# Performance work log

Measured on AMD Instinct MI355X. Metric: run time of the kernel, lower is better.

Reference implementation:

```python
import jax, jax.numpy as jnp
import numpy as np

B, L, F_, T = 64, 49, 2048, 32
V, E, H, A = 15000, 512, 512, 512

def _w(key, shape, scale=0.02):
    return (scale * jax.random.normal(key, shape)).astype(jnp.float32)

def setup_inputs() -> dict:
    key = jax.random.key(0)
    ks = jax.random.split(key, 24)
    inp = {
        "features": jax.random.normal(ks[0], (B, L, F_), dtype=jnp.float32),
        "captions": jax.random.randint(ks[1], (B, T), 0, V),
        "force_prob": 1,
        # parameters (torch nn.Linear convention: W [out,in])
        "init_h_W": _w(ks[2], (H, F_)), "init_h_b": jnp.zeros((H,), jnp.float32),
        "init_c_W": _w(ks[3], (H, F_)), "init_c_b": jnp.zeros((H,), jnp.float32),
        "W_a_W": _w(ks[4], (A, F_)), "W_a_b": jnp.zeros((A,), jnp.float32),
        "U_a_W": _w(ks[5], (A, H)), "U_a_b": jnp.zeros((A,), jnp.float32),
        "v_a_W": _w(ks[6], (1, A)), "v_a_b": jnp.zeros((1,), jnp.float32),
        "embed_table": _w(ks[7], (V, E), 1.0),
        "lstm_W_ih": _w(ks[8], (4 * H, E + F_)), "lstm_W_hh": _w(ks[9], (4 * H, H)),
        "lstm_b_ih": jnp.zeros((4 * H,), jnp.float32), "lstm_b_hh": jnp.zeros((4 * H,), jnp.float32),
        "fc_W": _w(ks[10], (V, H)), "fc_b": jnp.zeros((V,), jnp.float32),
    }
    return inp

def _decoder(features, captions,
             init_h_W, init_h_b, init_c_W, init_c_b,
             W_a_W, W_a_b, U_a_W, U_a_b, v_a_W, v_a_b,
             embed_table, lstm_W_ih, lstm_W_hh, lstm_b_ih, lstm_b_hh,
             fc_W, fc_b):
    emb = embed_table[captions]                      # [B,T,E]
    mean_f = jnp.mean(features, axis=1)              # [B,F]
    h0 = mean_f @ init_h_W.T + init_h_b              # [B,H]
    c0 = mean_f @ init_c_W.T + init_c_b
    # features are constant over time -> precompute W_a(features) once
    att1 = jnp.einsum('blf,af->bla', features, W_a_W) + W_a_b  # [B,L,A]

    def step(carry, w_emb):
        h, c = carry
        att2 = h @ U_a_W.T + U_a_b                   # [B,A]
        score = jnp.tanh(att1 + att2[:, None, :]) @ v_a_W[0] + v_a_b[0]  # [B,L]
        w = jax.nn.softmax(score, axis=1)            # [B,L]
        context = jnp.einsum('bl,blf->bf', w, features)  # [B,F]
        x = jnp.concatenate([w_emb, context], axis=1)     # [B,E+F]
        gates = x @ lstm_W_ih.T + lstm_b_ih + h @ lstm_W_hh.T + lstm_b_hh
        i, f, g, o = jnp.split(gates, 4, axis=1)
        i, f, o = jax.nn.sigmoid(i), jax.nn.sigmoid(f), jax.nn.sigmoid(o)
        g = jnp.tanh(g)
        c_new = f * c + i * g
        h_new = o * jnp.tanh(c_new)                  # dropout p=0 (eval) = identity
        logits = h_new @ fc_W.T + fc_b               # [B,V]
        return (h_new, c_new), logits

    _, logits = jax.lax.scan(step, (h0, c0), jnp.swapaxes(emb, 0, 1))  # [T,B,V]
    return jnp.transpose(logits, (1, 0, 2))          # [B,T,V]

def reference(features, captions, force_prob,
              init_h_W, init_h_b, init_c_W, init_c_b,
              W_a_W, W_a_b, U_a_W, U_a_b, v_a_W, v_a_b,
              embed_table, lstm_W_ih, lstm_W_hh, lstm_b_ih, lstm_b_hh,
              fc_W, fc_b):
    # force_prob == 1 -> teacher forcing at every step (sampling branch never taken)
    return _decoder(features, captions,
                    init_h_W, init_h_b, init_c_W, init_c_b,
                    W_a_W, W_a_b, U_a_W, U_a_b, v_a_W, v_a_b,
                    embed_table, lstm_W_ih, lstm_W_hh, lstm_b_ih, lstm_b_hh,
                    fc_W, fc_b)
```

## Files before the change

kernel.cpp:

```cpp
#include <hip/hip_runtime.h>
#include <math.h>

#define B_ 64
#define L_ 49
#define F_DIM 2048
#define T_ 32
#define V_ 15000
#define E_ 512
#define H_ 512
#define A_ 512

typedef __attribute__((ext_vector_type(8))) short s16x8;
typedef __attribute__((ext_vector_type(4))) short s16x4;
typedef __attribute__((ext_vector_type(4))) float f32x4;

__device__ __forceinline__ unsigned short f2b(float x) {
    union { float f; unsigned int u; } v; v.f = x;
    unsigned int r = v.u + 0x7FFF + ((v.u >> 16) & 1);
    return (unsigned short)(r >> 16);
}
__device__ __forceinline__ float b2f(unsigned short u) {
    union { unsigned int i; float f; } v; v.i = ((unsigned int)u) << 16; return v.f;
}
__device__ __forceinline__ float rcp_fast(float x) {
    return __builtin_amdgcn_rcpf(x);
}
__device__ __forceinline__ float tanhf_fast(float x) {
    x = fminf(fmaxf(x, -15.f), 15.f);
    const float e = __expf(2.f * x);
    return (e - 1.f) * rcp_fast(e + 1.f);
}
__device__ __forceinline__ float sigmoid_fast(float x) {
    return rcp_fast(1.f + __expf(-x));
}

__device__ __forceinline__ float aload_f(const float* p) {
    return __hip_atomic_load((const float*)p, __ATOMIC_RELAXED, __HIP_MEMORY_SCOPE_AGENT);
}
__device__ __forceinline__ void astore_f(float* p, float v) {
    __hip_atomic_store(p, v, __ATOMIC_RELAXED, __HIP_MEMORY_SCOPE_AGENT);
}
__device__ __forceinline__ unsigned long long aload_u64(const void* p) {
    return __hip_atomic_load((const unsigned long long*)p, __ATOMIC_RELAXED, __HIP_MEMORY_SCOPE_AGENT);
}
__device__ __forceinline__ void astore_u32(void* p, unsigned v) {
    __hip_atomic_store((unsigned*)p, v, __ATOMIC_RELAXED, __HIP_MEMORY_SCOPE_AGENT);
}
__device__ __forceinline__ unsigned apoll(const unsigned* p) {
    return __hip_atomic_load(p, __ATOMIC_RELAXED, __HIP_MEMORY_SCOPE_AGENT);
}
__device__ __forceinline__ void abump(unsigned* p) {
    __hip_atomic_fetch_add(p, 1u, __ATOMIC_RELAXED, __HIP_MEMORY_SCOPE_AGENT);
}
__device__ __forceinline__ void aset(unsigned* p, unsigned v) {
    __hip_atomic_store(p, v, __ATOMIC_RELAXED, __HIP_MEMORY_SCOPE_AGENT);
}

__global__ __launch_bounds__(256)
void k_castall(const float* __restrict__ feat, const float* __restrict__ W_a,
               const float* __restrict__ W_ih, const float* __restrict__ fc_W,
               unsigned short* __restrict__ feat_bf,
               unsigned short* __restrict__ wcomb_bf,
               unsigned short* __restrict__ fcW_bf)
{
    const int r  = blockIdx.y;
    const int c4 = blockIdx.x * 256 + threadIdx.x;
    const float* src;
    unsigned short* dst;
    int cols;
    if (r < 3136)      { src = feat + (size_t)r * 2048;                 dst = feat_bf + (size_t)r * 2048;            cols = 2048; }
    else if (r < 3648) { const int rr = r - 3136; src = W_a + (size_t)rr * 2048;              dst = wcomb_bf + (size_t)rr * 2048;          cols = 2048; }
    else if (r < 5696) { const int rr = r - 3648; src = W_ih + (size_t)rr * 2560 + 512;       dst = wcomb_bf + (size_t)(rr + 512) * 2048;  cols = 2048; }
    else               { const int rr = r - 5696; src = fc_W + (size_t)rr * 512;              dst = fcW_bf + (size_t)rr * 512;             cols = 512; }
    if (c4 * 4 >= cols) return;
    float4 v = *reinterpret_cast<const float4*>(src + c4 * 4);
    ushort4 o;
    o.x = f2b(v.x); o.y = f2b(v.y); o.z = f2b(v.z); o.w = f2b(v.w);
    *reinterpret_cast<ushort4*>(dst + c4 * 4) = o;
}

#define LDSW 40
__global__ __launch_bounds__(256)
void gemm_mfma(const unsigned short* __restrict__ A, int lda,
               const void* __restrict__ W0p, int ldw0, int N0,
               const void* __restrict__ W1p, int ldw1, int w32,
               const float* __restrict__ bias0, const float* __restrict__ bias1,
               float* __restrict__ C, int ldc,
               int M, int N, int K, int permT, int obf)
{
    __shared__ unsigned short As[128 * LDSW];
    __shared__ unsigned short Ws[128 * LDSW];

    const int tid  = threadIdx.x;
    const int m0   = blockIdx.x * 128;
    const int n0   = blockIdx.y * 128;
    const int wave = tid >> 6;
    const int lane = tid & 63;
    const int wr   = (wave >> 1) * 64;
    const int wc   = (wave & 1) * 64;

    f32x4 acc[4][4];
    #pragma unroll
    for (int i = 0; i < 4; ++i)
        #pragma unroll
        for (int j = 0; j < 4; ++j)
            acc[i][j] = (f32x4)(0.f);

    const int fr = lane & 15;
    const int fk = (lane >> 4) * 8;

    for (int kc = 0; kc < K; kc += 32) {
        ushort4 av[2][2], wv[2][2];
        #pragma unroll
        for (int i = 0; i < 2; ++i) {
            const int idx = tid + i * 256;
            const int row = idx >> 2;
            const int seg = idx & 3;
            av[i][0] = make_ushort4(0, 0, 0, 0); av[i][1] = make_ushort4(0, 0, 0, 0);
            wv[i][0] = make_ushort4(0, 0, 0, 0); wv[i][1] = make_ushort4(0, 0, 0, 0);
            if (m0 + row < M) {
                const float4 t0 = *reinterpret_cast<const float4*>(
                    A + (size_t)(m0 + row) * lda + kc + seg * 8);
                *reinterpret_cast<float4*>(&av[i][0]) = t0;
            }
            const int n_abs = n0 + row;
            if (n_abs < N) {
                if (w32) {
                    const float* wrow = (n_abs < N0)
                        ? ((const float*)W0p + (size_t)n_abs * ldw0)
                        : ((const float*)W1p + (size_t)(n_abs - N0) * ldw1);
                    const float4 x = *reinterpret_cast<const float4*>(wrow + kc + seg * 8);
                    const float4 y = *reinterpret_cast<const float4*>(wrow + kc + seg * 8 + 4);
                    wv[i][0] = make_ushort4(f2b(x.x), f2b(x.y), f2b(x.z), f2b(x.w));
                    wv[i][1] = make_ushort4(f2b(y.x), f2b(y.y), f2b(y.z), f2b(y.w));
                } else {
                    const unsigned short* wrow = (n_abs < N0)
                        ? ((const unsigned short*)W0p + (size_t)n_abs * ldw0)
                        : ((const unsigned short*)W1p + (size_t)(n_abs - N0) * ldw1);
                    const float4 t0 = *reinterpret_cast<const float4*>(wrow + kc + seg * 8);
                    *reinterpret_cast<float4*>(&wv[i][0]) = t0;
                }
            }
        }
        __syncthreads();
        #pragma unroll
        for (int i = 0; i < 2; ++i) {
            const int idx = tid + i * 256;
            const int row = idx >> 2;
            const int seg = idx & 3;
            *reinterpret_cast<ushort4*>(&As[row * LDSW + seg * 8])     = av[i][0];
            *reinterpret_cast<ushort4*>(&As[row * LDSW + seg * 8 + 4]) = av[i][1];
            *reinterpret_cast<ushort4*>(&Ws[row * LDSW + seg * 8])     = wv[i][0];
            *reinterpret_cast<ushort4*>(&Ws[row * LDSW + seg * 8 + 4]) = wv[i][1];
        }
        __syncthreads();

        s16x8 afr[4], bfr[4];
        #pragma unroll
        for (int mf = 0; mf < 4; ++mf)
            afr[mf] = *reinterpret_cast<const s16x8*>(&As[(wr + mf * 16 + fr) * LDSW + fk]);
        #pragma unroll
        for (int nf = 0; nf < 4; ++nf)
            bfr[nf] = *reinterpret_cast<const s16x8*>(&Ws[(wc + nf * 16 + fr) * LDSW + fk]);

        #pragma unroll
        for (int mf = 0; mf < 4; ++mf)
            #pragma unroll
            for (int nf = 0; nf < 4; ++nf)
                acc[mf][nf] = __builtin_amdgcn_mfma_f32_16x16x32_bf16(
                    afr[mf], bfr[nf], acc[mf][nf], 0, 0, 0);
    }

    const int cr = (lane >> 4) * 4;
    const int cc = lane & 15;
    #pragma unroll
    for (int nf = 0; nf < 4; ++nf) {
        const int n = n0 + wc + nf * 16 + cc;
        if (n >= N) continue;
        float bv = 0.f;
        if (bias0 && n < N0) bv += bias0[n];
        if (bias1) bv += bias1[n];
        #pragma unroll
        for (int mf = 0; mf < 4; ++mf) {
            #pragma unroll
            for (int r = 0; r < 4; ++r) {
                const int m = m0 + wr + mf * 16 + cr + r;
                if (m >= M) continue;
                const size_t row = permT ? ((size_t)(m & 63) * permT + (size_t)(m >> 6))
                                         : (size_t)m;
                const float v = acc[mf][nf][r] + bv;
                if (obf) ((unsigned short*)C)[row * (size_t)ldc + n] = f2b(v);
                else     C[row * (size_t)ldc + n] = v;
            }
        }
    }
}

__global__ __launch_bounds__(256)
void gemm64(const float* __restrict__ A, int lda,
            const float* __restrict__ W0, int ldw0, int N0,
            const float* __restrict__ W1, int ldw1,
            const float* __restrict__ bias0, const float* __restrict__ bias1,
            float* __restrict__ C, int ldc,
            int N, int K, int obf, float* __restrict__ C2)
{
    __shared__ float As[16][64];
    __shared__ float Ws[16][64];

    const int tid = threadIdx.x;
    const int m0  = blockIdx.x * 64;
    const int n0  = blockIdx.y * 64;

    const int lr = tid >> 2;
    const int kq = tid & 3;

    const int n_abs = n0 + lr;
    const bool wvalid = (n_abs < N);
    const float* wrow = nullptr;
    if (wvalid)
        wrow = (n_abs < N0) ? (W0 + (size_t)n_abs * ldw0)
                            : (W1 + (size_t)(n_abs - N0) * ldw1);
    const float* arow = A + (size_t)(m0 + lr) * lda;

    const int ty = tid >> 4;
    const int tx = tid & 15;

    float acc[4][4] = {{0.f}};

    for (int kc = 0; kc < K; kc += 16) {
        float4 av = *reinterpret_cast<const float4*>(arow + kc + kq * 4);
        float4 wv = make_float4(0.f, 0.f, 0.f, 0.f);
        if (wvalid)
            wv = *reinterpret_cast<const float4*>(wrow + kc + kq * 4);

        __syncthreads();
        As[kq * 4 + 0][lr] = av.x;
        As[kq * 4 + 1][lr] = av.y;
        As[kq * 4 + 2][lr] = av.z;
        As[kq * 4 + 3][lr] = av.w;
        Ws[kq * 4 + 0][lr] = wv.x;
        Ws[kq * 4 + 1][lr] = wv.y;
        Ws[kq * 4 + 2][lr] = wv.z;
        Ws[kq * 4 + 3][lr] = wv.w;
        __syncthreads();

        #pragma unroll
        for (int kk = 0; kk < 16; ++kk) {
            const float4 a4 = *reinterpret_cast<const float4*>(&As[kk][ty * 4]);
            const float4 w4 = *reinterpret_cast<const float4*>(&Ws[kk][tx * 4]);
            const float aa[4] = {a4.x, a4.y, a4.z, a4.w};
            const float ww[4] = {w4.x, w4.y, w4.z, w4.w};
            #pragma unroll
            for (int i = 0; i < 4; ++i)
                #pragma unroll
                for (int j = 0; j < 4; ++j)
                    acc[i][j] = fmaf(aa[i], ww[j], acc[i][j]);
        }
    }

    #pragma unroll
    for (int i = 0; i < 4; ++i) {
        const int m = m0 + ty * 4 + i;
        #pragma unroll
        for (int j = 0; j < 4; ++j) {
            const int n = n0 + tx * 4 + j;
            if (n >= N) continue;
            float v = acc[i][j];
            if (bias0 && n < N0) v += bias0[n];
            if (bias1 && n >= N0) v += bias1[n - N0];
            if (obf == 2) {
                if (n < N0) ((unsigned short*)C)[(size_t)m * N0 + n] = f2b(v);
                else        C2[(size_t)m * (N - N0) + (n - N0)] = v;
            } else if (obf == 1) {
                ((unsigned short*)C)[(size_t)m * ldc + n] = f2b(v);
            } else {
                C[(size_t)m * ldc + n] = v;
            }
        }
    }
}

__global__ __launch_bounds__(256)
void k_mean(const float* __restrict__ feat, float* __restrict__ mean_f)
{
    const int idx = blockIdx.x * 256 + threadIdx.x;
    const int b = idx >> 11;
    const int f = idx & 2047;
    const float* p = feat + (size_t)b * L_ * F_DIM + f;
    float s = 0.f;
    #pragma unroll 7
    for (int l = 0; l < L_; ++l) s += p[(size_t)l * F_DIM];
    mean_f[idx] = s * (1.0f / 49.0f);
}

__global__ __launch_bounds__(256)
void k_embgather(const float* __restrict__ table, const int* __restrict__ caps,
                 unsigned short* __restrict__ emb_bf)
{
    const int idx = blockIdx.x * 256 + threadIdx.x;
    const int e   = idx & 511;
    const int row = idx >> 9;
    const int t   = row >> 6;
    const int b   = row & 63;
    const int tok = caps[b * T_ + t];
    emb_bf[idx] = f2b(table[(size_t)tok * E_ + e]);
}

#define NBLK_RECUR 81u

__global__ __launch_bounds__(512)
void k_recur(unsigned short* __restrict__ hbf,
             float* __restrict__ att2g,
             const float* __restrict__ U_a,
             const float* __restrict__ W_hh,
             const float* __restrict__ U_a_b,
             const unsigned short* __restrict__ attFb,
             const float* __restrict__ g_emb,
             const float* __restrict__ v_w, const float* __restrict__ v_b,
             const float* __restrict__ c0,
             unsigned short* __restrict__ h_hist,
             unsigned* __restrict__ bar)
{
    const int g   = blockIdx.x;
    const int tid = threadIdx.x;

    if (g == 80) {
        if (tid == 0) {
            for (int t = 0; t < T_; ++t) {
                while (apoll(bar + 0) < (unsigned)(t * 64)) __builtin_amdgcn_s_sleep(1);
                #pragma unroll
                for (int i = 0; i < 8; ++i) aset(bar + 64 + i * 16, (unsigned)(t + 1));
                while (apoll(bar + 16) < (unsigned)((t + 1) * 16)) __builtin_amdgcn_s_sleep(1);
                #pragma unroll
                for (int i = 0; i < 8; ++i) aset(bar + 192 + i * 16, (unsigned)(t + 1));
                while (apoll(bar + 32) < (unsigned)((t + 1) * 80)) __builtin_amdgcn_s_sleep(1);
                #pragma unroll
                for (int i = 0; i < 8; ++i) aset(bar + 320 + i * 16, (unsigned)(t + 1));
            }
        }
        return;
    }

    __shared__ unsigned short Wc[32 * 520];
    __shared__ unsigned short hsd[64 * 520];
    __shared__ float a2[512];
    __shared__ float wl[64];
    __shared__ float gates[2048];
    __shared__ float hs[512];
    __shared__ float vws[512];
    __shared__ float vub[512];

    const int R    = g * 32;
    const int wave = tid >> 6;
    const int lane = tid & 63;
    const int grp  = g & 7;

    for (int idx = tid; idx < 4096; idx += 512) {
        const int r  = idx >> 7;
        const int kq = idx & 127;
        const int n  = R + r;
        const float* src = (n < 512) ? (U_a + (size_t)n * 512)
                                     : (W_hh + (size_t)(n - 512) * 512);
        float4 v = *reinterpret_cast<const float4*>(src + kq * 4);
        unsigned short* d = &Wc[r * 520 + kq * 4];
        d[0] = f2b(v.x); d[1] = f2b(v.y); d[2] = f2b(v.z); d[3] = f2b(v.w);
    }
    vws[tid] = v_w[tid];
    vub[tid] = U_a_b[tid];

    const int isB = (g < 64);
    const int b   = g;
    const float vb0 = v_b[0];

    const int ggrp = tid >> 7;
    const int jj   = (tid & 127) * 4;
    const int gc   = ggrp * 512 + jj;
    float creg = 0.f;
    if (isB) creg = c0[b * 512 + tid];

    const int tcol  = wave >> 2;
    const int rows0 = (wave & 3) * 16;
    const int frow  = lane & 15;
    const int fko   = (lane >> 4) * 8;
    __syncthreads();

    for (int t = 0; t < T_; ++t) {
        if (tid == 0)
            while (apoll(bar + 64 + grp * 16) < (unsigned)(t + 1)) __builtin_amdgcn_s_sleep(1);
        __syncthreads();

        {
            unsigned long long v[16];
            #pragma unroll
            for (int k = 0; k < 16; ++k)
                v[k] = aload_u64((const unsigned char*)hbf + ((size_t)(tid + k * 512)) * 8);
            #pragma unroll
            for (int k = 0; k < 16; ++k) {
                const int s   = tid + k * 512;
                const int row = s >> 7;
                const int c   = s & 127;
                *reinterpret_cast<unsigned long long*>(&hsd[row * 520 + c * 4]) = v[k];
            }
        }
        __syncthreads();

        {
            f32x4 acc = (f32x4)(0.f);
            #pragma unroll
            for (int ks = 0; ks < 16; ++ks) {
                const s16x8 af = *reinterpret_cast<const s16x8*>(
                    &hsd[(rows0 + frow) * 520 + ks * 32 + fko]);
                const s16x8 bf = *reinterpret_cast<const s16x8*>(
                    &Wc[(tcol * 16 + frow) * 520 + ks * 32 + fko]);
                acc = __builtin_amdgcn_mfma_f32_16x16x32_bf16(af, bf, acc, 0, 0, 0);
            }
            const int col = R + tcol * 16 + frow;
            #pragma unroll
            for (int r = 0; r < 4; ++r) {
                const int babs = rows0 + (lane >> 4) * 4 + r;
                astore_f(&att2g[(size_t)babs * 2560 + col], acc[r]);
            }
        }
        asm volatile("s_waitcnt vmcnt(0)" ::: "memory");
        __syncthreads();
        if (tid == 0) {
            if (g < 16) abump(bar + 16);
            abump(bar + 32);
        }

        if (isB) {
            if (tid == 0)
                while (apoll(bar + 192 + grp * 16) < (unsigned)(t + 1)) __builtin_amdgcn_s_sleep(1);
            __syncthreads();

            a2[tid] = aload_f(&att2g[(size_t)b * 2560 + tid]) + vub[tid];
            __syncthreads();

            for (int l = wave; l < L_; l += 8) {
                const s16x8 a1v = *reinterpret_cast<const s16x8*>(
                    attFb + (size_t)(b * L_ + l) * 2560 + lane * 8);
                float s = 0.f;
                #pragma unroll
                for (int j = 0; j < 8; ++j)
                    s += tanhf_fast(b2f((unsigned short)a1v[j]) + a2[lane * 8 + j]) * vws[lane * 8 + j];
                #pragma unroll
                for (int off = 32; off > 0; off >>= 1) s += __shfl_down(s, off);
                if (lane == 0) wl[l] = s + vb0;
            }
            __syncthreads();

            if (tid < 64) {
                float v = (tid < L_) ? wl[tid] : -3.0e38f;
                float mx = v;
                #pragma unroll
                for (int off = 32; off > 0; off >>= 1) mx = fmaxf(mx, __shfl_xor(mx, off));
                float e = (tid < L_) ? __expf(v - mx) : 0.f;
                float sum = e;
                #pragma unroll
                for (int off = 32; off > 0; off >>= 1) sum += __shfl_xor(sum, off);
                if (tid < L_) wl[tid] = e * rcp_fast(sum);
            }

            if (tid == 0)
                while (apoll(bar + 320 + grp * 16) < (unsigned)(t + 1)) __builtin_amdgcn_s_sleep(1);
            __syncthreads();

            {
                union { unsigned long long u; float f[2]; } q0, q1;
                q0.u = aload_u64(&att2g[(size_t)b * 2560 + 512 + gc]);
                q1.u = aload_u64(&att2g[(size_t)b * 2560 + 512 + gc + 2]);
                const float4 ge = *reinterpret_cast<const float4*>(
                    g_emb + ((size_t)t * 64 + b) * 2048 + gc);
                float s0 = ge.x + q0.f[0];
                float s1 = ge.y + q0.f[1];
                float s2 = ge.z + q1.f[0];
                float s3 = ge.w + q1.f[1];
                const unsigned short* fp = attFb + (size_t)(b * L_) * 2560 + 512 + gc;
                #pragma unroll 7
                for (int l = 0; l < L_; ++l) {
                    const float w = wl[l];
                    const s16x4 v = *reinterpret_cast<const s16x4*>(fp + (size_t)l * 2560);
                    s0 = fmaf(w, b2f((unsigned short)v[0]), s0);
                    s1 = fmaf(w, b2f((unsigned short)v[1]), s1);
                    s2 = fmaf(w, b2f((unsigned short)v[2]), s2);
                    s3 = fmaf(w, b2f((unsigned short)v[3]), s3);
                }
                *reinterpret_cast<float4*>(&gates[gc]) = make_float4(s0, s1, s2, s3);
            }
            __syncthreads();

            {
                const float gi = gates[tid],        gf = gates[512 + tid];
                const float gg = gates[1024 + tid], go = gates[1536 + tid];
                const float i = sigmoid_fast(gi);
                const float f = sigmoid_fast(gf);
                const float gv = tanhf_fast(gg);
                const float o = sigmoid_fast(go);
                creg = f * creg + i * gv;
                hs[tid] = o * tanhf_fast(creg);
            }
            __syncthreads();

            if (tid < 256) {
                const unsigned lo = f2b(hs[2 * tid]);
                const unsigned hi = f2b(hs[2 * tid + 1]);
                const unsigned pk = lo | (hi << 16);
                astore_u32((unsigned*)hbf + b * 256 + tid, pk);
                ((unsigned*)h_hist)[(size_t)(t * 64 + b) * 256 + tid] = pk;
            }
            asm volatile("s_waitcnt vmcnt(0)" ::: "memory");
            __syncthreads();
            if (tid == 0) abump(bar + 0);
        }
    }
}

extern "C" void kernel_launch(void* const* d_in, const int* in_sizes, int n_in,
                              void* d_out, int out_size, void* d_ws, size_t ws_size,
                              hipStream_t stream)
{
    const float* features = (const float*)d_in[0];
    const int*   captions = (const int*)d_in[1];
    const float* init_h_W = (const float*)d_in[3];
    const float* init_h_b = (const float*)d_in[4];
    const float* init_c_W = (const float*)d_in[5];
    const float* init_c_b = (const float*)d_in[6];
    const float* W_a_W    = (const float*)d_in[7];
    const float* W_a_b    = (const float*)d_in[8];
    const float* U_a_W    = (const float*)d_in[9];
    const float* U_a_b    = (const float*)d_in[10];
    const float* v_a_W    = (const float*)d_in[11];
    const float* v_a_b    = (const float*)d_in[12];
    const float* embed    = (const float*)d_in[13];
    const float* W_ih     = (const float*)d_in[14];
    const float* W_hh     = (const float*)d_in[15];
    const float* b_ih     = (const float*)d_in[16];
    const float* b_hh     = (const float*)d_in[17];
    const float* fc_W     = (const float*)d_in[18];
    const float* fc_b     = (const float*)d_in[19];
    float* out = (float*)d_out;

    float* ws      = (float*)d_ws;
    float* mean_f  = ws;
    float* c_st    = ws + 131072;
    unsigned short* h_bf   = (unsigned short*)(ws + 163840);
    unsigned short* h_hist = (unsigned short*)(ws + 180224);
    float* att2g   = ws + 704512;
    unsigned short* fcW_bf = (unsigned short*)(ws + 868352);
    unsigned* bar  = (unsigned*)(ws + 4708352);

    float* g_emb = out;
    unsigned short* attF_bf  = (unsigned short*)(out + 4194304);
    unsigned short* feat_bf  = (unsigned short*)(out + 13000000);
    unsigned short* wcomb_bf = (unsigned short*)(out + 17000000);
    unsigned short* emb_bf   = (unsigned short*)(out + 20000000);

    k_mean<<<512, 256, 0, stream>>>(features, mean_f);

    gemm64<<<dim3(1, 16), 256, 0, stream>>>(mean_f, F_DIM,
                                            init_h_W, F_DIM, H_,
                                            init_c_W, F_DIM,
                                            init_h_b, init_c_b,
                                            (float*)h_bf, H_, 2 * H_, F_DIM,
                                            2, c_st);

    k_embgather<<<4096, 256, 0, stream>>>(embed, captions, emb_bf);
    gemm_mfma<<<dim3(16, 16), 256, 0, stream>>>(emb_bf, E_,
                                                W_ih, E_ + F_DIM, 4 * H_,
                                                nullptr, 0, 1,
                                                b_ih, b_hh,
                                                g_emb, 4 * H_,
                                                2048, 4 * H_, E_, 0, 0);

    k_castall<<<dim3(2, 20696), 256, 0, stream>>>(features, W_a_W, W_ih, fc_W,
                                                  feat_bf, wcomb_bf, fcW_bf);

    gemm_mfma<<<dim3(25, 20), 256, 0, stream>>>(feat_bf, F_DIM,
                                                wcomb_bf, 2048, 512,
                                                wcomb_bf + (size_t)512 * 2048, 2048, 0,
                                                W_a_b, nullptr,
                                                (float*)attF_bf, 2560,
                                                3136, 2560, F_DIM, 0, 1);

    hipMemsetAsync(bar, 0, 4096, stream);
    k_recur<<<NBLK_RECUR, 512, 0, stream>>>(h_bf, att2g, U_a_W, W_hh, U_a_b,
                                            attF_bf, g_emb, v_a_W, v_a_b,
                                            c_st, h_hist, bar);

    gemm_mfma<<<dim3(16, 118), 256, 0, stream>>>(h_hist, H_,
                                                 fcW_bf, H_, V_,
                                                 nullptr, 0, 0,
                                                 fc_b, nullptr,
                                                 out, V_, 2048, V_, H_, 32, 0);
}
```

Measured before the change: 755.3 us.

## Replace coordinator-block barrier with per-block flag arrays polled by a wavefront

Removes the dedicated coordinator block that aggregated atomic counters and re-broadcast step flags. Each block now writes its own per-step flag slot, and consumers poll all producer flags in parallel with 64 lanes and a wave-wide vote. This cuts one relay hop from each of the three per-step synchronisation points in the serial 32-step recurrence. It also drops the t=0 wait. The cost is more polling traffic per waiting block and a larger barrier buffer to clear, which needs the workspace to be big enough.

```diff
diff --git a/kernel.cpp b/kernel.cpp
--- a/kernel.cpp
+++ b/kernel.cpp
@@ -48,9 +48,6 @@
 }
 __device__ __forceinline__ unsigned apoll(const unsigned* p) {
     return __hip_atomic_load(p, __ATOMIC_RELAXED, __HIP_MEMORY_SCOPE_AGENT);
-}
-__device__ __forceinline__ void abump(unsigned* p) {
-    __hip_atomic_fetch_add(p, 1u, __ATOMIC_RELAXED, __HIP_MEMORY_SCOPE_AGENT);
 }
 __device__ __forceinline__ void aset(unsigned* p, unsigned v) {
     __hip_atomic_store(p, v, __ATOMIC_RELAXED, __HIP_MEMORY_SCOPE_AGENT);
@@ -306,7 +303,7 @@
     emb_bf[idx] = f2b(table[(size_t)tok * E_ + e]);
 }
 
-#define NBLK_RECUR 81u
+#define NBLK_RECUR 80u
 
 __global__ __launch_bounds__(512)
 void k_recur(unsigned short* __restrict__ hbf,
@@ -324,23 +321,6 @@
     const int g   = blockIdx.x;
     const int tid = threadIdx.x;
 
-    if (g == 80) {
-        if (tid == 0) {
-            for (int t = 0; t < T_; ++t) {
-                while (apoll(bar + 0) < (unsigned)(t * 64)) __builtin_amdgcn_s_sleep(1);
-                #pragma unroll
-                for (int i = 0; i < 8; ++i) aset(bar + 64 + i * 16, (unsigned)(t + 1));
-                while (apoll(bar + 16) < (unsigned)((t + 1) * 16)) __builtin_amdgcn_s_sleep(1);
-                #pragma unroll
-                for (int i = 0; i < 8; ++i) aset(bar + 192 + i * 16, (unsigned)(t + 1));
-                while (apoll(bar + 32) < (unsigned)((t + 1) * 80)) __builtin_amdgcn_s_sleep(1);
-                #pragma unroll
-                for (int i = 0; i < 8; ++i) aset(bar + 320 + i * 16, (unsigned)(t + 1));
-            }
-        }
-        return;
-    }
-
     __shared__ unsigned short Wc[32 * 520];
     __shared__ unsigned short hsd[64 * 520];
     __shared__ float a2[512];
@@ -353,7 +333,6 @@
     const int R    = g * 32;
     const int wave = tid >> 6;
     const int lane = tid & 63;
-    const int grp  = g & 7;
 
     for (int idx = tid; idx < 4096; idx += 512) {
         const int r  = idx >> 7;
@@ -385,9 +364,13 @@
     __syncthreads();
 
     for (int t = 0; t < T_; ++t) {
-        if (tid == 0)
-            while (apoll(bar + 64 + grp * 16) < (unsigned)(t + 1)) __builtin_amdgcn_s_sleep(1);
-        __syncthreads();
+        if (t > 0) {
+            if (tid < 64) {
+                while (!__all((int)(apoll(bar + tid * 16) >= (unsigned)t)))
+                    __builtin_amdgcn_s_sleep(1);
+            }
+            __syncthreads();
+        }
 
         {
             unsigned long long v[16];
@@ -424,13 +407,16 @@
         asm volatile("s_waitcnt vmcnt(0)" ::: "memory");
         __syncthreads();
         if (tid == 0) {
-            if (g < 16) abump(bar + 16);
-            abump(bar + 32);
+            if (g < 16) aset(bar + 1024 + g * 16, (unsigned)(t + 1));
+            aset(bar + 1280 + g * 16, (unsigned)(t + 1));
         }
 
         if (isB) {
-            if (tid == 0)
-                while (apoll(bar + 192 + grp * 16) < (unsigned)(t + 1)) __builtin_amdgcn_s_sleep(1);
+            if (tid < 64) {
+                while (!__all((int)(tid >= 16 ||
+                        apoll(bar + 1024 + tid * 16) >= (unsigned)(t + 1))))
+                    __builtin_amdgcn_s_sleep(1);
+            }
             __syncthreads();
 
             a2[tid] = aload_f(&att2g[(size_t)b * 2560 + tid]) + vub[tid];
@@ -461,8 +447,15 @@
                 if (tid < L_) wl[tid] = e * rcp_fast(sum);
             }
 
-            if (tid == 0)
-                while (apoll(bar + 320 + grp * 16) < (unsigned)(t + 1)) __builtin_amdgcn_s_sleep(1);
+            if (tid < 64) {
+                for (;;) {
+                    const unsigned v0 = apoll(bar + 1280 + tid * 16);
+                    const unsigned v1 = (tid < 16) ? apoll(bar + 1280 + (tid + 64) * 16)
+                                                   : 0xFFFFFFFFu;
+                    if (__all((int)(v0 >= (unsigned)(t + 1) && v1 >= (unsigned)(t + 1)))) break;
+                    __builtin_amdgcn_s_sleep(1);
+                }
+            }
             __syncthreads();
 
             {
@@ -510,7 +503,7 @@
             }
             asm volatile("s_waitcnt vmcnt(0)" ::: "memory");
             __syncthreads();
-            if (tid == 0) abump(bar + 0);
+            if (tid == 0) aset(bar + b * 16, (unsigned)(t + 1));
         }
     }
 }
@@ -582,7 +575,7 @@
                                                 (float*)attF_bf, 2560,
                                                 3136, 2560, F_DIM, 0, 1);
 
-    hipMemsetAsync(bar, 0, 4096, stream);
+    hipMemsetAsync(bar, 0, 12288, stream);
     k_recur<<<NBLK_RECUR, 512, 0, stream>>>(h_bf, att2g, U_a_W, W_hh, U_a_b,
                                             attF_bf, g_emb, v_a_W, v_a_b,
                                             c_st, h_hist, bar);
```

Measured after the change: 744.4 us. No clear change (-1.4%).
